# Kernel optimization log

Measured on AMD Instinct MI355X. Metric: run time of the kernel, lower is better.

## Reference

```python
import jax, jax.numpy as jnp
import numpy as np

D_MODEL = 96
D_STATE = 16
D_CONV = 3
EXPAND = 2
D_INNER = D_MODEL * EXPAND          # 192
DT_RANK = max(1, D_MODEL // 16)     # 6
N_DIRS = 4
LN_EPS = 1e-5


def setup_inputs() -> dict:
    key = jax.random.key(0)
    ks = jax.random.split(key, 10)
    B, H, W = 2, 64, 64
    x = jax.random.normal(ks[0], (B, D_MODEL, H, W), dtype=jnp.float32)
    in_proj_w = jax.random.normal(ks[1], (2 * D_INNER, D_MODEL), dtype=jnp.float32) * 0.02
    conv_w = jax.random.normal(ks[2], (D_INNER, 1, D_CONV, D_CONV), dtype=jnp.float32) * 0.1
    conv_b = jnp.zeros((D_INNER,), dtype=jnp.float32)
    proj_dim = DT_RANK + 2 * D_STATE
    x_proj_weight = jax.random.normal(ks[3], (N_DIRS, D_INNER, proj_dim), dtype=jnp.float32) * 0.02
    dt_proj_weight = jax.random.normal(ks[4], (N_DIRS, D_INNER, DT_RANK), dtype=jnp.float32) * 0.02
    dt_proj_bias = jax.random.uniform(ks[5], (N_DIRS, D_INNER), dtype=jnp.float32) * 0.1
    A_log = jnp.log(jnp.broadcast_to(jnp.arange(1, D_STATE + 1, dtype=jnp.float32), (D_INNER, D_STATE)))
    D_skip = jnp.ones((D_INNER,), dtype=jnp.float32)
    ln_gamma = jnp.ones((D_INNER,), dtype=jnp.float32)
    ln_beta = jnp.zeros((D_INNER,), dtype=jnp.float32)
    out_proj_w = jax.random.normal(ks[6], (D_MODEL, D_INNER), dtype=jnp.float32) * 0.02
    return {
        "x": x, "in_proj_w": in_proj_w, "conv_w": conv_w, "conv_b": conv_b,
        "x_proj_weight": x_proj_weight, "dt_proj_weight": dt_proj_weight,
        "dt_proj_bias": dt_proj_bias, "A_log": A_log, "D_skip": D_skip,
        "ln_gamma": ln_gamma, "ln_beta": ln_beta, "out_proj_w": out_proj_w,
    }


def _ss2d_forward(x, in_proj_w, conv_w, conv_b, x_proj_weight, dt_proj_weight,
                  dt_proj_bias, A_log, D_skip, ln_gamma, ln_beta, out_proj_w):
    B, D, H, W = x.shape
    E, N, R = D_INNER, D_STATE, DT_RANK
    L = H * W
    # in_proj
    x_flat = x.reshape(B, D, L).transpose(0, 2, 1)              # b l d
    xz = x_flat @ in_proj_w.T                                    # b l 2e
    xb, z = xz[..., :E], xz[..., E:]
    # depthwise conv + SiLU
    xb = xb.transpose(0, 2, 1).reshape(B, E, H, W)
    xb = jax.lax.conv_general_dilated(
        xb, conv_w, window_strides=(1, 1), padding="SAME",
        feature_group_count=E, dimension_numbers=("NCHW", "OIHW", "NCHW"))
    xb = xb + conv_b[None, :, None, None]
    xb = jax.nn.silu(xb)
    # 4-directional cross-scan sequences
    x_rm = xb.reshape(B, E, L)
    x_cm = xb.transpose(0, 1, 3, 2).reshape(B, E, L)
    xs = jnp.stack([x_rm, x_rm[..., ::-1], x_cm, x_cm[..., ::-1]], axis=0)  # k b e l
    # per-direction projections
    x_for = xs.transpose(0, 1, 3, 2)                             # k b l e
    x_dbl = jnp.einsum("kble,ker->kblr", x_for, x_proj_weight)
    dt_low, Bs, Cs = x_dbl[..., :R], x_dbl[..., R:R + N], x_dbl[..., R + N:]
    dts = jnp.einsum("kblr,ker->kble", dt_low, dt_proj_weight) + dt_proj_bias[:, None, None, :]
    dt = jax.nn.softplus(dts)                                    # k b l e
    A = -jnp.exp(A_log)                                          # e n
    # batched selective scan over (k*b)
    KB = N_DIRS * B
    u = xs.reshape(KB, E, L)
    dt_ = dt.transpose(0, 1, 3, 2).reshape(KB, E, L)
    B_t = Bs.reshape(KB, L, N)
    C_t = Cs.reshape(KB, L, N)
    deltaA = jnp.exp(dt_[..., None] * A[None, :, None, :])       # kb e l n
    deltaBx = (dt_ * u)[..., None] * B_t[:, None, :, :]          # kb e l n

    def comb(c1, c2):
        a1, b1 = c1
        a2, b2 = c2
        return (a2 * a1, a2 * b1 + b2)

    _, h = jax.lax.associative_scan(comb, (deltaA, deltaBx), axis=2)  # kb e l n
    y = jnp.einsum("beln,bln->bel", h, C_t) + u * D_skip[None, :, None]
    ys = y.reshape(N_DIRS, B, E, L)
    y0, y1, y2, y3 = ys[0], ys[1][..., ::-1], ys[2], ys[3][..., ::-1]
    y_row = (y0 + y1).reshape(B, E, H, W)
    y_col = (y2 + y3).reshape(B, E, W, H).transpose(0, 1, 3, 2)
    yo = (y_row + y_col).reshape(B, E, L).transpose(0, 2, 1)     # b l e
    # LayerNorm over e
    mu = jnp.mean(yo, axis=-1, keepdims=True)
    var = jnp.mean((yo - mu) ** 2, axis=-1, keepdims=True)
    yo = (yo - mu) * jax.lax.rsqrt(var + LN_EPS) * ln_gamma + ln_beta
    yo = yo * jax.nn.silu(z)
    out = yo @ out_proj_w.T                                      # b l d
    return out.transpose(0, 2, 1).reshape(B, D, H, W)


def reference(x, in_proj_w, conv_w, conv_b, x_proj_weight, dt_proj_weight,
              dt_proj_bias, A_log, D_skip, ln_gamma, ln_beta, out_proj_w):
    return _ss2d_forward(x, in_proj_w, conv_w, conv_b, x_proj_weight,
                         dt_proj_weight, dt_proj_bias, A_log, D_skip,
                         ln_gamma, ln_beta, out_proj_w)
```

## Files before the change

kernel.cpp:

```cpp
#include <hip/hip_runtime.h>

#define LL 4096
#define HH 64
#define WWD 64
#define DM 96
#define EE 192
#define NN 16
#define RR 6
#define KBB 8
#define BB 2
#define CH 128
#define CLEN 32
#define SID (KBB * EE * NN)

__global__ __launch_bounds__(256) void k_inproj(const float* __restrict__ x,
                                                const float* __restrict__ W,
                                                float* __restrict__ xbuf,
                                                float* __restrict__ zbuf) {
    __shared__ __align__(16) float As[96][64];
    __shared__ __align__(16) float Ws[96][64];
    int bm = blockIdx.x;
    int bn = blockIdx.y;
    int l0 = bm * 64;
    int b  = l0 >> 12;
    int lb = l0 & (LL - 1);
    int j0 = bn * 64;
    int t  = threadIdx.x;

    for (int i = t; i < 96 * 16; i += 256) {
        int d = i >> 4, q = i & 15;
        *(float4*)&As[d][4 * q] = *(const float4*)&x[((size_t)b * 96 + d) * LL + lb + 4 * q];
    }
    for (int i = t; i < 96 * 64; i += 256) {
        int jn = i / 96, d = i - jn * 96;
        Ws[d][jn] = W[(size_t)(j0 + jn) * 96 + d];
    }
    __syncthreads();

    int tx = t & 15, ty = t >> 4;
    float acc[4][4] = {};
    for (int d = 0; d < 96; d++) {
        float4 av = *(const float4*)&As[d][ty * 4];
        float4 bv = *(const float4*)&Ws[d][tx * 4];
        float a[4] = {av.x, av.y, av.z, av.w};
        float bbv[4] = {bv.x, bv.y, bv.z, bv.w};
        for (int i = 0; i < 4; i++)
            for (int j = 0; j < 4; j++) acc[i][j] = fmaf(a[i], bbv[j], acc[i][j]);
    }
    for (int i = 0; i < 4; i++) {
        int l = lb + ty * 4 + i;
        for (int j = 0; j < 4; j++) {
            int jj = j0 + tx * 4 + j;
            if (jj < EE)
                xbuf[((size_t)b * EE + jj) * LL + l] = acc[i][j];
            else
                zbuf[((size_t)b * LL + l) * EE + (jj - EE)] = acc[i][j];
        }
    }
}

__global__ __launch_bounds__(256) void k_conv(const float* __restrict__ xbuf,
                                              const float* __restrict__ cw,
                                              const float* __restrict__ cb,
                                              float* __restrict__ xconv_t) {
    __shared__ float T[32][33];
    int l0 = blockIdx.x * 32;
    int e0 = blockIdx.y * 32;
    int b  = blockIdx.z;
    int t  = threadIdx.x;
    int tp = t & 31, teo = t >> 5;

    int pos = l0 + tp;
    int h = pos >> 6, w = pos & 63;
    #pragma unroll
    for (int j = 0; j < 4; j++) {
        int ee = j * 8 + teo;
        int e = e0 + ee;
        const float* src = xbuf + ((size_t)b * EE + e) * LL;
        const float* wgt = cw + e * 9;
        float acc = cb[e];
        #pragma unroll
        for (int dh = -1; dh <= 1; dh++) {
            int hh = h + dh;
            if (hh < 0 || hh >= HH) continue;
            #pragma unroll
            for (int dw = -1; dw <= 1; dw++) {
                int w2 = w + dw;
                if (w2 < 0 || w2 >= WWD) continue;
                acc = fmaf(src[hh * WWD + w2], wgt[(dh + 1) * 3 + (dw + 1)], acc);
            }
        }
        float v = acc / (1.f + __expf(-acc));
        T[ee][tp] = v;
    }
    __syncthreads();
    for (int i = t; i < 32 * 32; i += 256) {
        int p = i >> 5, ee = i & 31;
        xconv_t[((size_t)b * LL + l0 + p) * EE + e0 + ee] = T[ee][p];
    }
}

__device__ __forceinline__ int seq_of_spatial(int k, int idx) {
    if (k == 0) return idx;
    if (k == 1) return LL - 1 - idx;
    int p = ((idx & 63) << 6) | (idx >> 6);
    if (k == 2) return p;
    return LL - 1 - p;
}

__device__ __forceinline__ int spatial_of_seq(int k, int l) {
    int lp = (k & 1) ? (LL - 1 - l) : l;
    return (k >= 2) ? (((lp & 63) << 6) | (lp >> 6)) : lp;
}

__global__ __launch_bounds__(256, 2) void k_proj(const float* __restrict__ xconv_t,
                                                 const float* __restrict__ xpw,
                                                 const float* __restrict__ dtw,
                                                 const float* __restrict__ dtb,
                                                 float* __restrict__ dtbuf,
                                                 float* __restrict__ Bbuf,
                                                 float* __restrict__ Cbuf) {
    __shared__ __align__(16) float Ws[EE * 38 + 40];
    __shared__ __align__(16) float X[32][196];
    __shared__ float PR[32][8];
    __shared__ float BC[32][33];
    int l0 = blockIdx.x * 32;
    int b  = blockIdx.y;
    int k  = blockIdx.z;
    int t  = threadIdx.x;
    int pg = t >> 5;
    int oc = t & 31;

    const float* wsrc = xpw + (size_t)k * EE * 38;
    for (int i = t; i < (EE * 38) / 4; i += 256)
        ((float4*)Ws)[i] = ((const float4*)wsrc)[i];
    const float* xsrc = xconv_t + ((size_t)b * LL + l0) * EE;
    for (int i = t; i < (32 * EE) / 4; i += 256) {
        float4 v = ((const float4*)xsrc)[i];
        int pos = i / 48, e4 = i % 48;
        *(float4*)&X[pos][4 * e4] = v;
    }
    __syncthreads();

    int oc2 = oc + ((oc < 6) ? 32 : 0);

    float acc0[4] = {}, acc1[4] = {};
    #pragma unroll 2
    for (int e0 = 0; e0 < EE; e0 += 4) {
        float4 xv[4];
        #pragma unroll
        for (int ii = 0; ii < 4; ii++)
            xv[ii] = *(const float4*)&X[4 * pg + ii][e0];
        float w0[4], w1[4];
        #pragma unroll
        for (int j = 0; j < 4; j++) {
            w0[j] = Ws[(e0 + j) * 38 + oc];
            w1[j] = Ws[(e0 + j) * 38 + oc2];
        }
        #pragma unroll
        for (int ii = 0; ii < 4; ii++) {
            acc0[ii] = fmaf(xv[ii].x, w0[0], acc0[ii]);
            acc0[ii] = fmaf(xv[ii].y, w0[1], acc0[ii]);
            acc0[ii] = fmaf(xv[ii].z, w0[2], acc0[ii]);
            acc0[ii] = fmaf(xv[ii].w, w0[3], acc0[ii]);
            acc1[ii] = fmaf(xv[ii].x, w1[0], acc1[ii]);
            acc1[ii] = fmaf(xv[ii].y, w1[1], acc1[ii]);
            acc1[ii] = fmaf(xv[ii].z, w1[2], acc1[ii]);
            acc1[ii] = fmaf(xv[ii].w, w1[3], acc1[ii]);
        }
    }

    #pragma unroll
    for (int ii = 0; ii < 4; ii++) {
        int p = 4 * pg + ii;
        if (oc < 6) {
            PR[p][oc] = acc0[ii];
            BC[p][oc + 26] = acc1[ii];
        } else {
            BC[p][oc - 6] = acc0[ii];
        }
    }
    __syncthreads();

    int kb = k * 2 + b;
    for (int i = t; i < 32 * 32; i += 256) {
        int pos = i >> 5, c = i & 31;
        int j = seq_of_spatial(k, l0 + pos);
        float v = BC[pos][c];
        if (c < 16) Bbuf[((size_t)kb * LL + j) * NN + c] = v;
        else        Cbuf[((size_t)kb * LL + j) * NN + (c - 16)] = v;
    }

    for (int i = t; i < 32 * EE; i += 256) {
        int pos = i / EE;
        int e = i - pos * EE;
        float s = dtb[k * EE + e];
        const float* wr = dtw + ((size_t)k * EE + e) * RR;
        #pragma unroll
        for (int r = 0; r < RR; r++) s = fmaf(PR[pos][r], wr[r], s);
        float sp = (s > 20.f) ? s : log1pf(__expf(s));
        int j = seq_of_spatial(k, l0 + pos);
        dtbuf[((size_t)kb * LL + j) * EE + e] = sp;
    }
}

__global__ __launch_bounds__(192) void k_scan1(const float* __restrict__ xconv_t,
                                               const float* __restrict__ dtbuf,
                                               const float* __restrict__ Bbuf,
                                               const float* __restrict__ A_log,
                                               float* __restrict__ Ap,
                                               float* __restrict__ He) {
    __shared__ __align__(16) float sB[CLEN][NN];
    int c  = blockIdx.x;
    int kb = blockIdx.y;
    int k = kb >> 1, b = kb & 1;
    int e = threadIdx.x;
    int l0 = c * CLEN;

    for (int i = e; i < CLEN * NN; i += 192)
        ((float*)sB)[i] = Bbuf[((size_t)kb * LL + l0) * NN + i];

    float An[NN], h[NN], pa[NN];
    #pragma unroll
    for (int q = 0; q < 4; q++) {
        float4 al = *(const float4*)&A_log[e * NN + q * 4];
        An[q*4+0] = -__expf(al.x); An[q*4+1] = -__expf(al.y);
        An[q*4+2] = -__expf(al.z); An[q*4+3] = -__expf(al.w);
    }
    #pragma unroll
    for (int n = 0; n < NN; n++) { h[n] = 0.f; pa[n] = 1.f; }
    __syncthreads();

    const float* dtp = dtbuf + ((size_t)kb * LL + l0) * EE + e;
    const float* ub  = xconv_t + (size_t)b * LL * EE + e;

    #pragma unroll 2
    for (int i = 0; i < CLEN; i++) {
        int l = l0 + i;
        int idx = spatial_of_seq(k, l);
        float dtv = dtp[(size_t)i * EE];
        float u   = ub[(size_t)idx * EE];
        float Bv[NN];
        #pragma unroll
        for (int q = 0; q < 4; q++)
            *(float4*)&Bv[q*4] = ((const float4*)&sB[i][0])[q];
        float dtu = dtv * u;
        #pragma unroll
        for (int n = 0; n < NN; n++) {
            float a = __expf(dtv * An[n]);
            h[n] = fmaf(a, h[n], dtu * Bv[n]);
            pa[n] *= a;
        }
    }
    size_t sid = (size_t)c * SID + kb * (EE * NN) + e * NN;
    #pragma unroll
    for (int q = 0; q < 4; q++) {
        *(float4*)&Ap[sid + q*4] = make_float4(pa[q*4], pa[q*4+1], pa[q*4+2], pa[q*4+3]);
        *(float4*)&He[sid + q*4] = make_float4(h[q*4], h[q*4+1], h[q*4+2], h[q*4+3]);
    }
}

__global__ __launch_bounds__(256) void k_carry(float* __restrict__ ApHi,
                                               const float* __restrict__ He) {
    int sid = blockIdx.x * 256 + threadIdx.x;
    float h = 0.f;
    #pragma unroll 8
    for (int c = 0; c < CH; c++) {
        size_t ix = (size_t)c * SID + sid;
        float a  = ApHi[ix];
        float he = He[ix];
        ApHi[ix] = h;
        h = fmaf(a, h, he);
    }
}

__global__ __launch_bounds__(192) void k_scan2(const float* __restrict__ xconv_t,
                                               const float* __restrict__ dtbuf,
                                               const float* __restrict__ Bbuf,
                                               const float* __restrict__ Cbuf,
                                               const float* __restrict__ A_log,
                                               const float* __restrict__ Dskip,
                                               const float* __restrict__ Hi,
                                               float* __restrict__ ys) {
    __shared__ __align__(16) float sB[CLEN][NN];
    __shared__ __align__(16) float sC[CLEN][NN];
    int c  = blockIdx.x;
    int kb = blockIdx.y;
    int k = kb >> 1, b = kb & 1;
    int e = threadIdx.x;
    int l0 = c * CLEN;

    for (int i = e; i < CLEN * NN; i += 192) {
        ((float*)sB)[i] = Bbuf[((size_t)kb * LL + l0) * NN + i];
        ((float*)sC)[i] = Cbuf[((size_t)kb * LL + l0) * NN + i];
    }

    float An[NN], h[NN];
    #pragma unroll
    for (int q = 0; q < 4; q++) {
        float4 al = *(const float4*)&A_log[e * NN + q * 4];
        An[q*4+0] = -__expf(al.x); An[q*4+1] = -__expf(al.y);
        An[q*4+2] = -__expf(al.z); An[q*4+3] = -__expf(al.w);
    }
    size_t sid = (size_t)c * SID + kb * (EE * NN) + e * NN;
    #pragma unroll
    for (int q = 0; q < 4; q++) {
        float4 hv = *(const float4*)&Hi[sid + q*4];
        h[q*4+0] = hv.x; h[q*4+1] = hv.y; h[q*4+2] = hv.z; h[q*4+3] = hv.w;
    }
    float Dv = Dskip[e];
    __syncthreads();

    const float* dtp = dtbuf + ((size_t)kb * LL + l0) * EE + e;
    const float* ub  = xconv_t + (size_t)b * LL * EE + e;
    float* ysb       = ys + ((size_t)kb * LL + l0) * EE + e;

    #pragma unroll 2
    for (int i = 0; i < CLEN; i++) {
        int l = l0 + i;
        int idx = spatial_of_seq(k, l);
        float dtv = dtp[(size_t)i * EE];
        float u   = ub[(size_t)idx * EE];
        float Bv[NN], Cv[NN];
        #pragma unroll
        for (int q = 0; q < 4; q++) {
            *(float4*)&Bv[q*4] = ((const float4*)&sB[i][0])[q];
            *(float4*)&Cv[q*4] = ((const float4*)&sC[i][0])[q];
        }
        float dtu = dtv * u;
        float y = u * Dv;
        #pragma unroll
        for (int n = 0; n < NN; n++) {
            float a = __expf(dtv * An[n]);
            h[n] = fmaf(a, h[n], dtu * Bv[n]);
            y = fmaf(h[n], Cv[n], y);
        }
        ysb[(size_t)i * EE] = y;
    }
}

__global__ __launch_bounds__(256) void k_out(const float* __restrict__ ys,
                                             const float* __restrict__ zb,
                                             const float* __restrict__ gamma,
                                             const float* __restrict__ beta,
                                             const float* __restrict__ W2,
                                             float* __restrict__ out) {
    __shared__ __align__(16) float sbuf[32][196];
    int b  = blockIdx.x >> 7;
    int l0 = (blockIdx.x & 127) * 32;
    int t  = threadIdx.x;
    int wv = t >> 6, lane = t & 63;

    for (int li = 0; li < 32; li += 4) {
        int l = l0 + li + wv;
        int p = ((l & 63) << 6) | (l >> 6);
        const float* r0 = ys + ((size_t)(0 + b) * LL + l) * EE;
        const float* r1 = ys + ((size_t)(2 + b) * LL + (LL - 1 - l)) * EE;
        const float* r2 = ys + ((size_t)(4 + b) * LL + p) * EE;
        const float* r3 = ys + ((size_t)(6 + b) * LL + (LL - 1 - p)) * EE;
        const float* zrow = zb + ((size_t)b * LL + l) * EE;
        float v[3], zv[3];
        float s = 0.f;
        #pragma unroll
        for (int j = 0; j < 3; j++) {
            int e = lane + 64 * j;
            v[j] = r0[e] + r1[e] + r2[e] + r3[e];
            zv[j] = zrow[e];
            s += v[j];
        }
        for (int m = 1; m < 64; m <<= 1) s += __shfl_xor(s, m);
        float mu = s * (1.f / EE);
        float q = 0.f;
        #pragma unroll
        for (int j = 0; j < 3; j++) { float d = v[j] - mu; q = fmaf(d, d, q); }
        for (int m = 1; m < 64; m <<= 1) q += __shfl_xor(q, m);
        float rs = rsqrtf(q * (1.f / EE) + 1e-5f);
        #pragma unroll
        for (int j = 0; j < 3; j++) {
            int e = lane + 64 * j;
            float yn = (v[j] - mu) * rs * gamma[e] + beta[e];
            float zz = zv[j];
            float sil = zz / (1.f + __expf(-zz));
            sbuf[li + wv][e] = yn * sil;
        }
    }
    __syncthreads();
    for (int o = t; o < DM * 32; o += 256) {
        int d = o >> 5, c = o & 31;
        const float* wr = W2 + (size_t)d * EE;
        float acc = 0.f;
        for (int e = 0; e < EE; e += 4) {
            float4 sv = *(const float4*)&sbuf[c][e];
            float4 wv4 = *(const float4*)&wr[e];
            acc = fmaf(sv.x, wv4.x, acc);
            acc = fmaf(sv.y, wv4.y, acc);
            acc = fmaf(sv.z, wv4.z, acc);
            acc = fmaf(sv.w, wv4.w, acc);
        }
        out[((size_t)b * DM + d) * LL + l0 + c] = acc;
    }
}

extern "C" void kernel_launch(void* const* d_in, const int* in_sizes, int n_in,
                              void* d_out, int out_size, void* d_ws, size_t ws_size,
                              hipStream_t stream) {
    const float* x      = (const float*)d_in[0];
    const float* in_w   = (const float*)d_in[1];
    const float* conv_w = (const float*)d_in[2];
    const float* conv_b = (const float*)d_in[3];
    const float* xpw    = (const float*)d_in[4];
    const float* dtw    = (const float*)d_in[5];
    const float* dtbias = (const float*)d_in[6];
    const float* A_log  = (const float*)d_in[7];
    const float* Dsk    = (const float*)d_in[8];
    const float* gamma  = (const float*)d_in[9];
    const float* beta   = (const float*)d_in[10];
    const float* W2     = (const float*)d_in[11];
    float* out = (float*)d_out;

    float* ws      = (float*)d_ws;
    float* zbuf    = ws;
    float* xconv_t = zbuf    + (size_t)BB * LL * EE;
    float* dtbuf   = xconv_t + (size_t)BB * LL * EE;
    float* Bbuf    = dtbuf   + (size_t)KBB * LL * EE;
    float* Cbuf    = Bbuf    + (size_t)KBB * LL * NN;
    float* ApHi    = Cbuf    + (size_t)KBB * LL * NN;
    float* R       = ApHi    + (size_t)CH * SID;
    float* ys      = R;
    float* xbuf    = R;
    float* He      = R + 2 * (size_t)BB * EE * LL;

    k_inproj<<<dim3(128, 6), 256, 0, stream>>>(x, in_w, xbuf, zbuf);
    k_conv<<<dim3(128, 6, 2), 256, 0, stream>>>(xbuf, conv_w, conv_b, xconv_t);
    k_proj<<<dim3(128, 2, 4), 256, 0, stream>>>(xconv_t, xpw, dtw, dtbias, dtbuf, Bbuf, Cbuf);
    k_scan1<<<dim3(CH, KBB), 192, 0, stream>>>(xconv_t, dtbuf, Bbuf, A_log, ApHi, He);
    k_carry<<<SID / 256, 256, 0, stream>>>(ApHi, He);
    k_scan2<<<dim3(CH, KBB), 192, 0, stream>>>(xconv_t, dtbuf, Bbuf, Cbuf, A_log, Dsk, ApHi, ys);
    k_out<<<BB * (LL / 32), 256, 0, stream>>>(ys, zbuf, gamma, beta, W2, out);
}
```

Measured before the change: 269.0 us.

## Store in_proj output as a single row-major xz buffer and simplify conv/proj

The in_proj kernel now writes x and z together into one position-major buffer with 384 columns using float4 stores, replacing the scattered channel-major writes to xbuf. The conv kernel is restructured so each thread handles one channel across 8 columns of a row, reading the row-major xz directly and writing xconv_t without a shared-memory transpose. k_proj transposes its weight tile in shared memory so weights load as float4. The aim is to remove strided global stores and the transpose step. In exchange, the conv kernel reads 9 taps per output with stride 384 and no reuse through shared memory, and the workspace for xz grows.

```diff
diff --git a/kernel.cpp b/kernel.cpp
--- a/kernel.cpp
+++ b/kernel.cpp
@@ -12,11 +12,11 @@
 #define CH 128
 #define CLEN 32
 #define SID (KBB * EE * NN)
+#define XZP 384
 
 __global__ __launch_bounds__(256) void k_inproj(const float* __restrict__ x,
                                                 const float* __restrict__ W,
-                                                float* __restrict__ xbuf,
-                                                float* __restrict__ zbuf) {
+                                                float* __restrict__ xz) {
     __shared__ __align__(16) float As[96][64];
     __shared__ __align__(16) float Ws[96][64];
     int bm = blockIdx.x;
@@ -49,36 +49,32 @@
     }
     for (int i = 0; i < 4; i++) {
         int l = lb + ty * 4 + i;
-        for (int j = 0; j < 4; j++) {
-            int jj = j0 + tx * 4 + j;
-            if (jj < EE)
-                xbuf[((size_t)b * EE + jj) * LL + l] = acc[i][j];
-            else
-                zbuf[((size_t)b * LL + l) * EE + (jj - EE)] = acc[i][j];
-        }
-    }
-}
-
-__global__ __launch_bounds__(256) void k_conv(const float* __restrict__ xbuf,
+        float* orow = xz + ((size_t)b * LL + l) * XZP + j0 + tx * 4;
+        *(float4*)orow = make_float4(acc[i][0], acc[i][1], acc[i][2], acc[i][3]);
+    }
+}
+
+__global__ __launch_bounds__(192) void k_conv(const float* __restrict__ xz,
                                               const float* __restrict__ cw,
                                               const float* __restrict__ cb,
                                               float* __restrict__ xconv_t) {
-    __shared__ float T[32][33];
-    int l0 = blockIdx.x * 32;
-    int e0 = blockIdx.y * 32;
+    int wq = blockIdx.x;
+    int h  = blockIdx.y;
     int b  = blockIdx.z;
-    int t  = threadIdx.x;
-    int tp = t & 31, teo = t >> 5;
-
-    int pos = l0 + tp;
-    int h = pos >> 6, w = pos & 63;
-    #pragma unroll
-    for (int j = 0; j < 4; j++) {
-        int ee = j * 8 + teo;
-        int e = e0 + ee;
-        const float* src = xbuf + ((size_t)b * EE + e) * LL;
-        const float* wgt = cw + e * 9;
-        float acc = cb[e];
+    int e  = threadIdx.x;
+
+    float wgt[9];
+    #pragma unroll
+    for (int i = 0; i < 9; i++) wgt[i] = cw[e * 9 + i];
+    float bias = cb[e];
+
+    const float* base = xz + (size_t)b * LL * XZP + e;
+    float* outb = xconv_t + (size_t)b * LL * EE + e;
+
+    #pragma unroll
+    for (int wi = 0; wi < 8; wi++) {
+        int w = wq * 8 + wi;
+        float acc = bias;
         #pragma unroll
         for (int dh = -1; dh <= 1; dh++) {
             int hh = h + dh;
@@ -87,16 +83,10 @@
             for (int dw = -1; dw <= 1; dw++) {
                 int w2 = w + dw;
                 if (w2 < 0 || w2 >= WWD) continue;
-                acc = fmaf(src[hh * WWD + w2], wgt[(dh + 1) * 3 + (dw + 1)], acc);
+                acc = fmaf(base[(size_t)(hh * 64 + w2) * XZP], wgt[(dh + 1) * 3 + (dw + 1)], acc);
             }
         }
-        float v = acc / (1.f + __expf(-acc));
-        T[ee][tp] = v;
-    }
-    __syncthreads();
-    for (int i = t; i < 32 * 32; i += 256) {
-        int p = i >> 5, ee = i & 31;
-        xconv_t[((size_t)b * LL + l0 + p) * EE + e0 + ee] = T[ee][p];
+        outb[(size_t)(h * 64 + w) * EE] = acc / (1.f + __expf(-acc));
     }
 }
 
@@ -120,7 +110,7 @@
                                                  float* __restrict__ dtbuf,
                                                  float* __restrict__ Bbuf,
                                                  float* __restrict__ Cbuf) {
-    __shared__ __align__(16) float Ws[EE * 38 + 40];
+    __shared__ __align__(16) float Wt[38][196];
     __shared__ __align__(16) float X[32][196];
     __shared__ float PR[32][8];
     __shared__ float BC[32][33];
@@ -132,8 +122,10 @@
     int oc = t & 31;
 
     const float* wsrc = xpw + (size_t)k * EE * 38;
-    for (int i = t; i < (EE * 38) / 4; i += 256)
-        ((float4*)Ws)[i] = ((const float4*)wsrc)[i];
+    for (int i = t; i < EE * 38; i += 256) {
+        int e = i / 38, col = i - e * 38;
+        Wt[col][e] = wsrc[i];
+    }
     const float* xsrc = xconv_t + ((size_t)b * LL + l0) * EE;
     for (int i = t; i < (32 * EE) / 4; i += 256) {
         float4 v = ((const float4*)xsrc)[i];
@@ -142,7 +134,7 @@
     }
     __syncthreads();
 
-    int oc2 = oc + ((oc < 6) ? 32 : 0);
+    int oc2 = (oc < 6) ? (oc + 32) : oc;
 
     float acc0[4] = {}, acc1[4] = {};
     #pragma unroll 2
@@ -151,22 +143,18 @@
         #pragma unroll
         for (int ii = 0; ii < 4; ii++)
             xv[ii] = *(const float4*)&X[4 * pg + ii][e0];
-        float w0[4], w1[4];
-        #pragma unroll
-        for (int j = 0; j < 4; j++) {
-            w0[j] = Ws[(e0 + j) * 38 + oc];
-            w1[j] = Ws[(e0 + j) * 38 + oc2];
-        }
+        float4 w0 = *(const float4*)&Wt[oc][e0];
+        float4 w1 = *(const float4*)&Wt[oc2][e0];
         #pragma unroll
         for (int ii = 0; ii < 4; ii++) {
-            acc0[ii] = fmaf(xv[ii].x, w0[0], acc0[ii]);
-            acc0[ii] = fmaf(xv[ii].y, w0[1], acc0[ii]);
-            acc0[ii] = fmaf(xv[ii].z, w0[2], acc0[ii]);
-            acc0[ii] = fmaf(xv[ii].w, w0[3], acc0[ii]);
-            acc1[ii] = fmaf(xv[ii].x, w1[0], acc1[ii]);
-            acc1[ii] = fmaf(xv[ii].y, w1[1], acc1[ii]);
-            acc1[ii] = fmaf(xv[ii].z, w1[2], acc1[ii]);
-            acc1[ii] = fmaf(xv[ii].w, w1[3], acc1[ii]);
+            acc0[ii] = fmaf(xv[ii].x, w0.x, acc0[ii]);
+            acc0[ii] = fmaf(xv[ii].y, w0.y, acc0[ii]);
+            acc0[ii] = fmaf(xv[ii].z, w0.z, acc0[ii]);
+            acc0[ii] = fmaf(xv[ii].w, w0.w, acc0[ii]);
+            acc1[ii] = fmaf(xv[ii].x, w1.x, acc1[ii]);
+            acc1[ii] = fmaf(xv[ii].y, w1.y, acc1[ii]);
+            acc1[ii] = fmaf(xv[ii].z, w1.z, acc1[ii]);
+            acc1[ii] = fmaf(xv[ii].w, w1.w, acc1[ii]);
         }
     }
 
@@ -340,7 +328,7 @@
 }
 
 __global__ __launch_bounds__(256) void k_out(const float* __restrict__ ys,
-                                             const float* __restrict__ zb,
+                                             const float* __restrict__ xz,
                                              const float* __restrict__ gamma,
                                              const float* __restrict__ beta,
                                              const float* __restrict__ W2,
@@ -358,7 +346,7 @@
         const float* r1 = ys + ((size_t)(2 + b) * LL + (LL - 1 - l)) * EE;
         const float* r2 = ys + ((size_t)(4 + b) * LL + p) * EE;
         const float* r3 = ys + ((size_t)(6 + b) * LL + (LL - 1 - p)) * EE;
-        const float* zrow = zb + ((size_t)b * LL + l) * EE;
+        const float* zrow = xz + ((size_t)b * LL + l) * XZP + EE;
         float v[3], zv[3];
         float s = 0.f;
         #pragma unroll
@@ -419,22 +407,21 @@
     float* out = (float*)d_out;
 
     float* ws      = (float*)d_ws;
-    float* zbuf    = ws;
-    float* xconv_t = zbuf    + (size_t)BB * LL * EE;
+    float* xz      = ws;
+    float* xconv_t = xz      + (size_t)BB * LL * XZP;
     float* dtbuf   = xconv_t + (size_t)BB * LL * EE;
     float* Bbuf    = dtbuf   + (size_t)KBB * LL * EE;
     float* Cbuf    = Bbuf    + (size_t)KBB * LL * NN;
     float* ApHi    = Cbuf    + (size_t)KBB * LL * NN;
     float* R       = ApHi    + (size_t)CH * SID;
     float* ys      = R;
-    float* xbuf    = R;
     float* He      = R + 2 * (size_t)BB * EE * LL;
 
-    k_inproj<<<dim3(128, 6), 256, 0, stream>>>(x, in_w, xbuf, zbuf);
-    k_conv<<<dim3(128, 6, 2), 256, 0, stream>>>(xbuf, conv_w, conv_b, xconv_t);
+    k_inproj<<<dim3(128, 6), 256, 0, stream>>>(x, in_w, xz);
+    k_conv<<<dim3(8, 64, 2), 192, 0, stream>>>(xz, conv_w, conv_b, xconv_t);
     k_proj<<<dim3(128, 2, 4), 256, 0, stream>>>(xconv_t, xpw, dtw, dtbias, dtbuf, Bbuf, Cbuf);
     k_scan1<<<dim3(CH, KBB), 192, 0, stream>>>(xconv_t, dtbuf, Bbuf, A_log, ApHi, He);
     k_carry<<<SID / 256, 256, 0, stream>>>(ApHi, He);
     k_scan2<<<dim3(CH, KBB), 192, 0, stream>>>(xconv_t, dtbuf, Bbuf, Cbuf, A_log, Dsk, ApHi, ys);
-    k_out<<<BB * (LL / 32), 256, 0, stream>>>(ys, zbuf, gamma, beta, W2, out);
-}
+    k_out<<<BB * (LL / 32), 256, 0, stream>>>(ys, xz, gamma, beta, W2, out);
+}
```

Result: no change. 270.5 us (+0.6%).
